# Kernel optimization log

Hardware: AMD Instinct MI355X
Metric: run time of the kernel (lower is better)

Reference implementation:

```python
import jax, jax.numpy as jnp
import numpy as np

N = 100000      # nodes
E = 3200000     # edges (before self loops)
IN = 128        # in_channels
H = 8           # heads
C = 16          # out_channels per head
NEG_SLOPE = 0.2


def setup_inputs() -> dict:
    key = jax.random.key(0)
    k1, k2, k3, k4, k5, k6 = jax.random.split(key, 6)
    x = jax.random.normal(k1, (N, IN), dtype=jnp.float32)
    edge_index = jax.random.randint(k2, (2, E), 0, N, dtype=jnp.int32)
    # GATConv params: lin weight [IN, H*C], att_src/att_dst [H, C], bias [H*C]
    W = jax.random.normal(k3, (IN, H * C), dtype=jnp.float32) / np.float32(np.sqrt(IN))
    att_src = jax.random.normal(k4, (H, C), dtype=jnp.float32) / np.float32(np.sqrt(C))
    att_dst = jax.random.normal(k5, (H, C), dtype=jnp.float32) / np.float32(np.sqrt(C))
    bias = jax.random.normal(k6, (H * C,), dtype=jnp.float32) * 0.01
    return {"x": x, "edge_index": edge_index, "W": W,
            "att_src": att_src, "att_dst": att_dst, "bias": bias}


def reference(x, edge_index, W, att_src, att_dst, bias):
    n = x.shape[0]
    h = (x @ W).reshape(n, H, C)                      # [N, H, C]
    # add self loops (PyG default add_self_loops=True)
    loop = jnp.arange(n, dtype=edge_index.dtype)
    src = jnp.concatenate([edge_index[0], loop])      # [E+N] message sources j
    dst = jnp.concatenate([edge_index[1], loop])      # [E+N] targets i
    # per-node attention logits
    a_src = jnp.einsum('nhc,hc->nh', h, att_src)      # [N, H]
    a_dst = jnp.einsum('nhc,hc->nh', h, att_dst)      # [N, H]
    alpha = jax.nn.leaky_relu(a_src[src] + a_dst[dst], NEG_SLOPE)  # [E+N, H]
    # segment softmax over edges grouped by destination node
    amax = jax.lax.stop_gradient(jax.ops.segment_max(alpha, dst, num_segments=n))
    ex = jnp.exp(alpha - amax[dst])
    denom = jax.ops.segment_sum(ex, dst, num_segments=n)           # [N, H]
    w = ex / (denom[dst] + 1e-16)                                  # [E+N, H]
    msg = h[src] * w[:, :, None]                                   # [E+N, H, C]
    out = jax.ops.segment_sum(msg, dst, num_segments=n)            # [N, H, C]
    return out.reshape(n, H * C) + bias
```

## Files before the change

### kernel.cpp

```cpp
#include <hip/hip_runtime.h>
#include <hip/hip_bf16.h>

#define H 8
#define C 16
#define HC 128
#define NEG 0.2f
#define XS_S 132

#define ANSH 6
#define AN 64
#define AMSK 63
#define CAP2 2560
#define MAXB2 2048
#define CB_SH 12
#define CBMSK 4095
#define MAXB1 64
#define EPB 4096

__device__ __forceinline__ float lrelu(float x) { return fmaxf(x, NEG * x); }

__device__ __forceinline__ unsigned pack_bf16(float a, float b) {
    union { __hip_bfloat16 h; unsigned short u; } ua, ub;
    ua.h = __float2bfloat16(a);
    ub.h = __float2bfloat16(b);
    return (unsigned)ua.u | ((unsigned)ub.u << 16);
}
__device__ __forceinline__ float bf_lo(unsigned d) { return __uint_as_float(d << 16); }
__device__ __forceinline__ float bf_hi(unsigned d) { return __uint_as_float(d & 0xffff0000u); }

__global__ void __launch_bounds__(256) k1_gemm(const float* __restrict__ x,
                                               const float* __restrict__ W,
                                               const float* __restrict__ att_src,
                                               const float* __restrict__ att_dst,
                                               unsigned* __restrict__ h16,
                                               float* __restrict__ a_src,
                                               float* __restrict__ a_dst, int N) {
    __shared__ float xs[64 * XS_S];
    const int n0 = blockIdx.x * 64;
    const int t = threadIdx.x;
#pragma unroll
    for (int i = 0; i < 8; ++i) {
        int id = t + 256 * i;
        int r = id >> 5, kq = id & 31;
        int n = n0 + r;
        float4 v = (n < N) ? ((const float4*)x)[(size_t)n * 32 + kq]
                           : make_float4(0.f, 0.f, 0.f, 0.f);
        *(float4*)&xs[r * XS_S + kq * 4] = v;
    }
    __syncthreads();
    const int cg = t & 31;
    const int r0 = (t >> 5) * 8;
    float acc[8][4];
#pragma unroll
    for (int i = 0; i < 8; ++i)
#pragma unroll
        for (int j = 0; j < 4; ++j) acc[i][j] = 0.f;

#pragma unroll 4
    for (int k = 0; k < HC; ++k) {
        const float4 wv = ((const float4*)W)[k * 32 + cg];
        float wr[4] = {wv.x, wv.y, wv.z, wv.w};
#pragma unroll
        for (int i = 0; i < 8; ++i) {
            float xv = xs[(r0 + i) * XS_S + k];
#pragma unroll
            for (int j = 0; j < 4; ++j) acc[i][j] += xv * wr[j];
        }
    }
    const int fhd = cg >> 2;
    const int cq  = cg & 3;
#pragma unroll
    for (int i = 0; i < 8; ++i) {
        int n = n0 + r0 + i;
        if (n < N) {
            uint2 dv = make_uint2(pack_bf16(acc[i][0], acc[i][1]),
                                  pack_bf16(acc[i][2], acc[i][3]));
            *(uint2*)&h16[(size_t)n * 64 + cg * 2] = dv;
        }
        float ps = 0.f, pd = 0.f;
#pragma unroll
        for (int jj = 0; jj < 4; ++jj) {
            float hv = acc[i][jj];
            ps += hv * att_src[fhd * C + cq * 4 + jj];
            pd += hv * att_dst[fhd * C + cq * 4 + jj];
        }
        ps += __shfl_xor(ps, 1, 4); pd += __shfl_xor(pd, 1, 4);
        ps += __shfl_xor(ps, 2, 4); pd += __shfl_xor(pd, 2, 4);
        if (cq == 0 && n < N) {
            a_src[(unsigned)n * 8u + fhd] = ps;
            a_dst[(unsigned)n * 8u + fhd] = pd;
        }
    }
}

__global__ void __launch_bounds__(256) kb_bin1(const int* __restrict__ ei,
                                               int* __restrict__ gcount1,
                                               unsigned* __restrict__ pairs1,
                                               int E, int NB1, int cap1) {
    __shared__ int hist[4][MAXB1];
    __shared__ int cur[4][MAXB1];
    __shared__ int tot[MAXB1];
    __shared__ int scn[MAXB1];
    const int t = threadIdx.x;
    const int wv = t >> 6;
    const int e0 = blockIdx.x * EPB;
    const int nE = min(EPB, E - e0);
    ((int*)hist)[t] = 0;
    __syncthreads();

    const bool al4 = ((E & 3) == 0);
    const int nE4 = nE >> 2;
    int4 dreg[4], sreg[4];
    const int4* d4p = (const int4*)(ei + E + e0);
    const int4* s4p = (const int4*)(ei + e0);
#pragma unroll
    for (int j = 0; j < 4; ++j) {
        int idx = j * 256 + t;
        if (idx < nE4) {
            if (al4) { dreg[j] = d4p[idx]; sreg[j] = s4p[idx]; }
            else {
                int e = idx * 4;
                dreg[j] = make_int4(ei[E + e0 + e], ei[E + e0 + e + 1],
                                    ei[E + e0 + e + 2], ei[E + e0 + e + 3]);
                sreg[j] = make_int4(ei[e0 + e], ei[e0 + e + 1],
                                    ei[e0 + e + 2], ei[e0 + e + 3]);
            }
        }
    }
    int tlD = 0, tlS = -1;
    {
        int tb = nE4 * 4 + t;
        if (tb < nE) { tlD = ei[E + e0 + tb]; tlS = ei[e0 + tb]; }
    }
#pragma unroll
    for (int j = 0; j < 4; ++j) {
        if (j * 256 + t < nE4) {
            atomicAdd(&hist[wv][dreg[j].x >> CB_SH], 1);
            atomicAdd(&hist[wv][dreg[j].y >> CB_SH], 1);
            atomicAdd(&hist[wv][dreg[j].z >> CB_SH], 1);
            atomicAdd(&hist[wv][dreg[j].w >> CB_SH], 1);
        }
    }
    if (tlS >= 0) atomicAdd(&hist[wv][tlD >> CB_SH], 1);
    __syncthreads();
    if (t < MAXB1) {
        int s = 0;
#pragma unroll
        for (int w = 0; w < 4; ++w) s += hist[w][t];
        tot[t] = s;
        scn[t] = s;
    }
    __syncthreads();
    for (int off = 1; off < MAXB1; off <<= 1) {
        int v = (t < MAXB1 && t >= off) ? scn[t - off] : 0;
        __syncthreads();
        if (t < MAXB1) scn[t] += v;
        __syncthreads();
    }
    if (t < MAXB1) {
        int h = tot[t];
        int gb = h ? t * cap1 + atomicAdd(&gcount1[t], h) : 0;
#pragma unroll
        for (int w = 0; w < 4; ++w) { cur[w][t] = gb; gb += hist[w][t]; }
    }
    __syncthreads();
#pragma unroll
    for (int j = 0; j < 4; ++j) {
        if (j * 256 + t < nE4) {
#pragma unroll
            for (int q = 0; q < 4; ++q) {
                int dst = (&dreg[j].x)[q], src = (&sreg[j].x)[q];
                int b = dst >> CB_SH;
                int pos = atomicAdd(&cur[wv][b], 1);
                if (pos < b * cap1 + cap1)
                    pairs1[pos] = (unsigned)src | ((unsigned)(dst & CBMSK) << 17);
            }
        }
    }
    if (tlS >= 0) {
        int b = tlD >> CB_SH;
        int pos = atomicAdd(&cur[wv][b], 1);
        if (pos < b * cap1 + cap1)
            pairs1[pos] = (unsigned)tlS | ((unsigned)(tlD & CBMSK) << 17);
    }
}

__global__ void __launch_bounds__(256) kb_bin2(const unsigned* __restrict__ pairs1,
                                               const int* __restrict__ gcount1,
                                               int* __restrict__ gcount2,
                                               unsigned* __restrict__ pairs2,
                                               int cap1, int ch2) {
    __shared__ int hist[4][64];
    __shared__ int cur[4][64];
    __shared__ int tot[64];
    const int cb = blockIdx.x / ch2;
    const int ci = blockIdx.x % ch2;
    const int c1 = min(gcount1[cb], cap1);
    const int e0 = ci * EPB;
    if (e0 >= c1) return;
    const int nE = min(EPB, c1 - e0);
    const unsigned b1 = (unsigned)cb * (unsigned)cap1 + (unsigned)e0;
    const int t = threadIdx.x;
    const int wv = t >> 6;
    ((int*)hist)[t] = 0;
    __syncthreads();

    const int nE4 = nE >> 2;
    const uint4* p4 = (const uint4*)(pairs1 + b1);
    uint4 preg[4];
#pragma unroll
    for (int j = 0; j < 4; ++j) {
        int idx = j * 256 + t;
        if (idx < nE4) preg[j] = p4[idx];
    }
    unsigned tlP = 0; int tlV = 0;
    {
        int tb = nE4 * 4 + t;
        if (tb < nE) { tlP = pairs1[b1 + tb]; tlV = 1; }
    }
#pragma unroll
    for (int j = 0; j < 4; ++j) {
        if (j * 256 + t < nE4) {
            atomicAdd(&hist[wv][preg[j].x >> 23], 1);
            atomicAdd(&hist[wv][preg[j].y >> 23], 1);
            atomicAdd(&hist[wv][preg[j].z >> 23], 1);
            atomicAdd(&hist[wv][preg[j].w >> 23], 1);
        }
    }
    if (tlV) atomicAdd(&hist[wv][tlP >> 23], 1);
    __syncthreads();
    if (t < 64) {
        int s = 0;
#pragma unroll
        for (int w = 0; w < 4; ++w) s += hist[w][t];
        tot[t] = s;
    }
    __syncthreads();
    if (t < 64) {
        int h = tot[t];
        int gfb = cb * 64 + t;
        int gb = h ? gfb * CAP2 + atomicAdd(&gcount2[gfb], h) : 0;
#pragma unroll
        for (int w = 0; w < 4; ++w) { cur[w][t] = gb; gb += hist[w][t]; }
    }
    __syncthreads();
#pragma unroll
    for (int j = 0; j < 4; ++j) {
        if (j * 256 + t < nE4) {
#pragma unroll
            for (int q = 0; q < 4; ++q) {
                unsigned pv = (&preg[j].x)[q];
                int fb = pv >> 23;
                int pos = atomicAdd(&cur[wv][fb], 1);
                if (pos < (cb * 64 + fb) * CAP2 + CAP2)
                    pairs2[pos] = (pv & 0x1FFFFu) | (((pv >> 17) & 63u) << 18);
            }
        }
    }
    if (tlV) {
        int fb = tlP >> 23;
        int pos = atomicAdd(&cur[wv][fb], 1);
        if (pos < (cb * 64 + fb) * CAP2 + CAP2)
            pairs2[pos] = (tlP & 0x1FFFFu) | (((tlP >> 17) & 63u) << 18);
    }
}

__global__ void __launch_bounds__(512) k_fused(const unsigned* __restrict__ pairs,
                                               const int* __restrict__ gcount,
                                               const unsigned* __restrict__ h16,
                                               const float* __restrict__ a_src,
                                               const float* __restrict__ a_dst,
                                               const float* __restrict__ bias,
                                               float* __restrict__ out, int N) {
    __shared__ int cnt[AN];
    __shared__ int sc[AN];
    __shared__ int lcur[AN];
    __shared__ int lbeg[AN + 1];
    __shared__ unsigned scol[CAP2];
    const int b = blockIdx.x;
    const int t = threadIdx.x;
    const int n0 = b << ANSH;
    const unsigned base = (unsigned)b * (unsigned)CAP2;
    const int cb = min(gcount[b], CAP2);

    if (t < AN) cnt[t] = 0;
    __syncthreads();
    for (int j = t; j < cb; j += 512)
        atomicAdd(&cnt[pairs[base + j] >> 18], 1);
    __syncthreads();
    if (t < AN) sc[t] = cnt[t];
    __syncthreads();
    for (int off = 1; off < AN; off <<= 1) {
        int v = (t < AN && t >= off) ? sc[t - off] : 0;
        __syncthreads();
        if (t < AN) sc[t] += v;
        __syncthreads();
    }
    if (t < AN) {
        lbeg[t + 1] = sc[t];
        lcur[t] = sc[t] - cnt[t];
        if (t == 0) lbeg[0] = 0;
    }
    __syncthreads();
    for (int j = t; j < cb; j += 512) {
        unsigned pv = pairs[base + j];
        int pos = atomicAdd(&lcur[pv >> 18], 1);
        scol[pos] = pv & 0x3FFFFu;
    }
    __syncthreads();

    const int wv = t >> 6;
    const int lane = t & 63;
    const int hd = lane >> 3;
    const int hw = lane & 7;
    const int bidx = hd * 4;

    for (int nl = wv; nl < AN; nl += 8) {
        const int node = n0 + nl;
        if (node >= N) break;
        const float adst_own = a_dst[(unsigned)node * 8u + (unsigned)hd];
        const float adst_hh  = a_dst[(unsigned)node * 8u + (unsigned)hw];
        const float wself = __expf(lrelu(a_src[(unsigned)node * 8u + (unsigned)hd] + adst_own));
        unsigned dself = h16[(unsigned)node * 64u + (unsigned)lane];
        float a0 = bf_lo(dself) * wself, a1 = bf_hi(dself) * wself;
        float b0 = 0.f, b1 = 0.f, c0 = 0.f, c1 = 0.f, e0 = 0.f, e1 = 0.f;
        float sA = wself, sB = 0.f, sC = 0.f, sD = 0.f;

        const int beg = lbeg[nl], end = lbeg[nl + 1];
        int j = beg;
        for (; j + 8 <= end; j += 8) {
            unsigned m0 = scol[j],     m1 = scol[j + 1], m2 = scol[j + 2], m3 = scol[j + 3];
            unsigned m4 = scol[j + 4], m5 = scol[j + 5], m6 = scol[j + 6], m7 = scol[j + 7];
            unsigned nP = scol[j + (lane >> 3)];
            float wme = __expf(lrelu(a_src[nP * 8u + (unsigned)hw] + adst_hh));
            int wi = __float_as_int(wme);
            float w0 = __int_as_float(__builtin_amdgcn_ds_bpermute(bidx,       wi));
            float w1 = __int_as_float(__builtin_amdgcn_ds_bpermute(bidx + 32,  wi));
            float w2 = __int_as_float(__builtin_amdgcn_ds_bpermute(bidx + 64,  wi));
            float w3 = __int_as_float(__builtin_amdgcn_ds_bpermute(bidx + 96,  wi));
            float w4 = __int_as_float(__builtin_amdgcn_ds_bpermute(bidx + 128, wi));
            float w5 = __int_as_float(__builtin_amdgcn_ds_bpermute(bidx + 160, wi));
            float w6 = __int_as_float(__builtin_amdgcn_ds_bpermute(bidx + 192, wi));
            float w7 = __int_as_float(__builtin_amdgcn_ds_bpermute(bidx + 224, wi));
            unsigned d0 = h16[m0 * 64u + (unsigned)lane];
            unsigned d1 = h16[m1 * 64u + (unsigned)lane];
            unsigned d2 = h16[m2 * 64u + (unsigned)lane];
            unsigned d3 = h16[m3 * 64u + (unsigned)lane];
            unsigned d4 = h16[m4 * 64u + (unsigned)lane];
            unsigned d5 = h16[m5 * 64u + (unsigned)lane];
            unsigned d6 = h16[m6 * 64u + (unsigned)lane];
            unsigned d7 = h16[m7 * 64u + (unsigned)lane];
            a0 += bf_lo(d0) * w0; a1 += bf_hi(d0) * w0; sA += w0;
            b0 += bf_lo(d1) * w1; b1 += bf_hi(d1) * w1; sB += w1;
            c0 += bf_lo(d2) * w2; c1 += bf_hi(d2) * w2; sC += w2;
            e0 += bf_lo(d3) * w3; e1 += bf_hi(d3) * w3; sD += w3;
            a0 += bf_lo(d4) * w4; a1 += bf_hi(d4) * w4; sA += w4;
            b0 += bf_lo(d5) * w5; b1 += bf_hi(d5) * w5; sB += w5;
            c0 += bf_lo(d6) * w6; c1 += bf_hi(d6) * w6; sC += w6;
            e0 += bf_lo(d7) * w7; e1 += bf_hi(d7) * w7; sD += w7;
        }
        if (j + 4 <= end) {
            unsigned m0 = scol[j], m1 = scol[j + 1], m2 = scol[j + 2], m3 = scol[j + 3];
            unsigned nP = scol[j + ((lane >> 3) & 3)];
            float wme = __expf(lrelu(a_src[nP * 8u + (unsigned)hw] + adst_hh));
            int wi = __float_as_int(wme);
            float w0 = __int_as_float(__builtin_amdgcn_ds_bpermute(bidx,      wi));
            float w1 = __int_as_float(__builtin_amdgcn_ds_bpermute(bidx + 32, wi));
            float w2 = __int_as_float(__builtin_amdgcn_ds_bpermute(bidx + 64, wi));
            float w3 = __int_as_float(__builtin_amdgcn_ds_bpermute(bidx + 96, wi));
            unsigned d0 = h16[m0 * 64u + (unsigned)lane];
            unsigned d1 = h16[m1 * 64u + (unsigned)lane];
            unsigned d2 = h16[m2 * 64u + (unsigned)lane];
            unsigned d3 = h16[m3 * 64u + (unsigned)lane];
            a0 += bf_lo(d0) * w0; a1 += bf_hi(d0) * w0; sA += w0;
            b0 += bf_lo(d1) * w1; b1 += bf_hi(d1) * w1; sB += w1;
            c0 += bf_lo(d2) * w2; c1 += bf_hi(d2) * w2; sC += w2;
            e0 += bf_lo(d3) * w3; e1 += bf_hi(d3) * w3; sD += w3;
            j += 4;
        }
        for (; j < end; ++j) {
            unsigned mA = scol[j];
            float wA = __expf(lrelu(a_src[mA * 8u + (unsigned)hd] + adst_own));
            unsigned dA = h16[mA * 64u + (unsigned)lane];
            a0 += bf_lo(dA) * wA; a1 += bf_hi(dA) * wA; sA += wA;
        }
        const float s = sA + sB + sC + sD;
        const float inv = 1.f / (s + 1e-16f);
        const float acc0 = a0 + b0 + c0 + e0;
        const float acc1 = a1 + b1 + c1 + e1;
        const float2 bv = ((const float2*)bias)[lane];
        float2 o;
        o.x = acc0 * inv + bv.x;
        o.y = acc1 * inv + bv.y;
        ((float2*)out)[(unsigned)node * 64u + (unsigned)lane] = o;
    }
}

extern "C" void kernel_launch(void* const* d_in, const int* in_sizes, int n_in,
                              void* d_out, int out_size, void* d_ws, size_t ws_size,
                              hipStream_t stream) {
    const float* x       = (const float*)d_in[0];
    const int*   ei      = (const int*)d_in[1];
    const float* W       = (const float*)d_in[2];
    const float* att_src = (const float*)d_in[3];
    const float* att_dst = (const float*)d_in[4];
    const float* bias    = (const float*)d_in[5];
    float* out = (float*)d_out;

    const int N = in_sizes[0] / HC;
    const int E = in_sizes[1] / 2;
    const int B = (N + AMSK) >> ANSH;
    const int NB1 = (N + CBMSK) >> CB_SH;
    const int nbin = (E + EPB - 1) / EPB;
    const int cap1 = (((E + NB1 - 1) / NB1) + 32768 + 3) & ~3;
    const int ch2 = (cap1 + EPB - 1) / EPB;

    unsigned* h16 = (unsigned*)d_ws;
    float* a_src  = (float*)(h16 + (size_t)N * 64);
    float* a_dst  = a_src + (size_t)N * H;
    int* gcount1  = (int*)(a_dst + (size_t)N * H);
    int* gcount2  = gcount1 + MAXB1;
    unsigned* pairs1 = (unsigned*)(gcount2 + MAXB2);
    unsigned* pairs2 = pairs1 + (size_t)NB1 * (size_t)cap1;

    (void)hipMemsetAsync(gcount1, 0, (MAXB1 + MAXB2) * sizeof(int), stream);
    kb_bin1<<<nbin, 256, 0, stream>>>(ei, gcount1, pairs1, E, NB1, cap1);
    kb_bin2<<<NB1 * ch2, 256, 0, stream>>>(pairs1, gcount1, gcount2, pairs2,
                                           cap1, ch2);
    k1_gemm<<<(N + 63) / 64, 256, 0, stream>>>(x, W, att_src, att_dst,
                                               h16, a_src, a_dst, N);
    k_fused<<<B, 512, 0, stream>>>(pairs2, gcount2, h16, a_src,
                                   a_dst, bias, out, N);
}
```

Measured before the change: 353.9 us.

## Sub-bucket edges by source range and aggregate in phases for gather locality

Within each destination block, edges are now counted and sorted by (destination node, source range of 16K nodes) with a 512-entry scan, then processed in eight phases separated by block barriers. Each phase gathers only h16 rows from one source range, so concurrent blocks touch a smaller working set and L2 hit rates may rise. Partial sums are kept in shared memory (an added 32KB float2 tile plus per-head sums) and finalized in a last pass with the self-loop term. The cost is eight extra barriers, a larger scan, shorter per-segment loops with a 4-wide unroll in place of 8, and higher LDS use, which may lower occupancy.

Result: slower. 426.7 us (+20.6%).

```diff
diff --git a/kernel.cpp b/kernel.cpp
--- a/kernel.cpp
+++ b/kernel.cpp
@@ -16,6 +16,8 @@
 #define CBMSK 4095
 #define MAXB1 64
 #define EPB 4096
+#define NTL 8
+#define TL_SH 14
 
 __device__ __forceinline__ float lrelu(float x) { return fmaxf(x, NEG * x); }
 
@@ -272,39 +274,42 @@
                                                const float* __restrict__ a_dst,
                                                const float* __restrict__ bias,
                                                float* __restrict__ out, int N) {
-    __shared__ int cnt[AN];
-    __shared__ int sc[AN];
-    __shared__ int lcur[AN];
-    __shared__ int lbeg[AN + 1];
+    __shared__ int cnt[AN * NTL];
+    __shared__ int sc[AN * NTL];
+    __shared__ int lcur[AN * NTL];
     __shared__ unsigned scol[CAP2];
+    __shared__ float2 st[AN * 64];
+    __shared__ float ssum[AN * 8];
     const int b = blockIdx.x;
     const int t = threadIdx.x;
     const int n0 = b << ANSH;
     const unsigned base = (unsigned)b * (unsigned)CAP2;
     const int cb = min(gcount[b], CAP2);
 
-    if (t < AN) cnt[t] = 0;
-    __syncthreads();
-    for (int j = t; j < cb; j += 512)
-        atomicAdd(&cnt[pairs[base + j] >> 18], 1);
-    __syncthreads();
-    if (t < AN) sc[t] = cnt[t];
-    __syncthreads();
-    for (int off = 1; off < AN; off <<= 1) {
-        int v = (t < AN && t >= off) ? sc[t - off] : 0;
-        __syncthreads();
-        if (t < AN) sc[t] += v;
-        __syncthreads();
-    }
-    if (t < AN) {
-        lbeg[t + 1] = sc[t];
-        lcur[t] = sc[t] - cnt[t];
-        if (t == 0) lbeg[0] = 0;
-    }
+    cnt[t] = 0;
+    ssum[t] = 0.f;
+    for (int i = t; i < AN * 64; i += 512) st[i] = make_float2(0.f, 0.f);
     __syncthreads();
     for (int j = t; j < cb; j += 512) {
         unsigned pv = pairs[base + j];
-        int pos = atomicAdd(&lcur[pv >> 18], 1);
+        int key = (int)((pv >> 18) * NTL + ((pv & 0x3FFFFu) >> TL_SH));
+        atomicAdd(&cnt[key], 1);
+    }
+    __syncthreads();
+    sc[t] = cnt[t];
+    __syncthreads();
+    for (int off = 1; off < AN * NTL; off <<= 1) {
+        int v = (t >= off) ? sc[t - off] : 0;
+        __syncthreads();
+        sc[t] += v;
+        __syncthreads();
+    }
+    lcur[t] = sc[t] - cnt[t];
+    __syncthreads();
+    for (int j = t; j < cb; j += 512) {
+        unsigned pv = pairs[base + j];
+        int key = (int)((pv >> 18) * NTL + ((pv & 0x3FFFFu) >> TL_SH));
+        int pos = atomicAdd(&lcur[key], 1);
         scol[pos] = pv & 0x3FFFFu;
     }
     __syncthreads();
@@ -315,83 +320,63 @@
     const int hw = lane & 7;
     const int bidx = hd * 4;
 
+    for (int s = 0; s < NTL; ++s) {
+        for (int nl = wv; nl < AN; nl += 8) {
+            const int key = nl * NTL + s;
+            const int beg = key ? sc[key - 1] : 0;
+            const int end = sc[key];
+            const int node = n0 + nl;
+            if (beg >= end || node >= N) continue;
+            float2 stv = st[nl * 64 + lane];
+            float sacc = 0.f;
+            const float adst_own = a_dst[(unsigned)node * 8u + (unsigned)hd];
+            const float adst_hh  = a_dst[(unsigned)node * 8u + (unsigned)hw];
+            int j = beg;
+            for (; j + 4 <= end; j += 4) {
+                unsigned m0 = scol[j], m1 = scol[j + 1];
+                unsigned m2 = scol[j + 2], m3 = scol[j + 3];
+                unsigned nP = scol[j + ((lane >> 3) & 3)];
+                float wme = __expf(lrelu(a_src[nP * 8u + (unsigned)hw] + adst_hh));
+                int wi = __float_as_int(wme);
+                float w0 = __int_as_float(__builtin_amdgcn_ds_bpermute(bidx,      wi));
+                float w1 = __int_as_float(__builtin_amdgcn_ds_bpermute(bidx + 32, wi));
+                float w2 = __int_as_float(__builtin_amdgcn_ds_bpermute(bidx + 64, wi));
+                float w3 = __int_as_float(__builtin_amdgcn_ds_bpermute(bidx + 96, wi));
+                unsigned d0 = h16[m0 * 64u + (unsigned)lane];
+                unsigned d1 = h16[m1 * 64u + (unsigned)lane];
+                unsigned d2 = h16[m2 * 64u + (unsigned)lane];
+                unsigned d3 = h16[m3 * 64u + (unsigned)lane];
+                stv.x += bf_lo(d0) * w0; stv.y += bf_hi(d0) * w0;
+                stv.x += bf_lo(d1) * w1; stv.y += bf_hi(d1) * w1;
+                stv.x += bf_lo(d2) * w2; stv.y += bf_hi(d2) * w2;
+                stv.x += bf_lo(d3) * w3; stv.y += bf_hi(d3) * w3;
+                sacc += w0 + w1 + w2 + w3;
+            }
+            for (; j < end; ++j) {
+                unsigned mA = scol[j];
+                float wA = __expf(lrelu(a_src[mA * 8u + (unsigned)hd] + adst_own));
+                unsigned dA = h16[mA * 64u + (unsigned)lane];
+                stv.x += bf_lo(dA) * wA; stv.y += bf_hi(dA) * wA;
+                sacc += wA;
+            }
+            st[nl * 64 + lane] = stv;
+            if ((lane & 7) == 0) ssum[nl * 8 + hd] += sacc;
+        }
+        __syncthreads();
+    }
+
     for (int nl = wv; nl < AN; nl += 8) {
         const int node = n0 + nl;
-        if (node >= N) break;
-        const float adst_own = a_dst[(unsigned)node * 8u + (unsigned)hd];
-        const float adst_hh  = a_dst[(unsigned)node * 8u + (unsigned)hw];
-        const float wself = __expf(lrelu(a_src[(unsigned)node * 8u + (unsigned)hd] + adst_own));
-        unsigned dself = h16[(unsigned)node * 64u + (unsigned)lane];
-        float a0 = bf_lo(dself) * wself, a1 = bf_hi(dself) * wself;
-        float b0 = 0.f, b1 = 0.f, c0 = 0.f, c1 = 0.f, e0 = 0.f, e1 = 0.f;
-        float sA = wself, sB = 0.f, sC = 0.f, sD = 0.f;
-
-        const int beg = lbeg[nl], end = lbeg[nl + 1];
-        int j = beg;
-        for (; j + 8 <= end; j += 8) {
-            unsigned m0 = scol[j],     m1 = scol[j + 1], m2 = scol[j + 2], m3 = scol[j + 3];
-            unsigned m4 = scol[j + 4], m5 = scol[j + 5], m6 = scol[j + 6], m7 = scol[j + 7];
-            unsigned nP = scol[j + (lane >> 3)];
-            float wme = __expf(lrelu(a_src[nP * 8u + (unsigned)hw] + adst_hh));
-            int wi = __float_as_int(wme);
-            float w0 = __int_as_float(__builtin_amdgcn_ds_bpermute(bidx,       wi));
-            float w1 = __int_as_float(__builtin_amdgcn_ds_bpermute(bidx + 32,  wi));
-            float w2 = __int_as_float(__builtin_amdgcn_ds_bpermute(bidx + 64,  wi));
-            float w3 = __int_as_float(__builtin_amdgcn_ds_bpermute(bidx + 96,  wi));
-            float w4 = __int_as_float(__builtin_amdgcn_ds_bpermute(bidx + 128, wi));
-            float w5 = __int_as_float(__builtin_amdgcn_ds_bpermute(bidx + 160, wi));
-            float w6 = __int_as_float(__builtin_amdgcn_ds_bpermute(bidx + 192, wi));
-            float w7 = __int_as_float(__builtin_amdgcn_ds_bpermute(bidx + 224, wi));
-            unsigned d0 = h16[m0 * 64u + (unsigned)lane];
-            unsigned d1 = h16[m1 * 64u + (unsigned)lane];
-            unsigned d2 = h16[m2 * 64u + (unsigned)lane];
-            unsigned d3 = h16[m3 * 64u + (unsigned)lane];
-            unsigned d4 = h16[m4 * 64u + (unsigned)lane];
-            unsigned d5 = h16[m5 * 64u + (unsigned)lane];
-            unsigned d6 = h16[m6 * 64u + (unsigned)lane];
-            unsigned d7 = h16[m7 * 64u + (unsigned)lane];
-            a0 += bf_lo(d0) * w0; a1 += bf_hi(d0) * w0; sA += w0;
-            b0 += bf_lo(d1) * w1; b1 += bf_hi(d1) * w1; sB += w1;
-            c0 += bf_lo(d2) * w2; c1 += bf_hi(d2) * w2; sC += w2;
-            e0 += bf_lo(d3) * w3; e1 += bf_hi(d3) * w3; sD += w3;
-            a0 += bf_lo(d4) * w4; a1 += bf_hi(d4) * w4; sA += w4;
-            b0 += bf_lo(d5) * w5; b1 += bf_hi(d5) * w5; sB += w5;
-            c0 += bf_lo(d6) * w6; c1 += bf_hi(d6) * w6; sC += w6;
-            e0 += bf_lo(d7) * w7; e1 += bf_hi(d7) * w7; sD += w7;
-        }
-        if (j + 4 <= end) {
-            unsigned m0 = scol[j], m1 = scol[j + 1], m2 = scol[j + 2], m3 = scol[j + 3];
-            unsigned nP = scol[j + ((lane >> 3) & 3)];
-            float wme = __expf(lrelu(a_src[nP * 8u + (unsigned)hw] + adst_hh));
-            int wi = __float_as_int(wme);
-            float w0 = __int_as_float(__builtin_amdgcn_ds_bpermute(bidx,      wi));
-            float w1 = __int_as_float(__builtin_amdgcn_ds_bpermute(bidx + 32, wi));
-            float w2 = __int_as_float(__builtin_amdgcn_ds_bpermute(bidx + 64, wi));
-            float w3 = __int_as_float(__builtin_amdgcn_ds_bpermute(bidx + 96, wi));
-            unsigned d0 = h16[m0 * 64u + (unsigned)lane];
-            unsigned d1 = h16[m1 * 64u + (unsigned)lane];
-            unsigned d2 = h16[m2 * 64u + (unsigned)lane];
-            unsigned d3 = h16[m3 * 64u + (unsigned)lane];
-            a0 += bf_lo(d0) * w0; a1 += bf_hi(d0) * w0; sA += w0;
-            b0 += bf_lo(d1) * w1; b1 += bf_hi(d1) * w1; sB += w1;
-            c0 += bf_lo(d2) * w2; c1 += bf_hi(d2) * w2; sC += w2;
-            e0 += bf_lo(d3) * w3; e1 += bf_hi(d3) * w3; sD += w3;
-            j += 4;
-        }
-        for (; j < end; ++j) {
-            unsigned mA = scol[j];
-            float wA = __expf(lrelu(a_src[mA * 8u + (unsigned)hd] + adst_own));
-            unsigned dA = h16[mA * 64u + (unsigned)lane];
-            a0 += bf_lo(dA) * wA; a1 += bf_hi(dA) * wA; sA += wA;
-        }
-        const float s = sA + sB + sC + sD;
-        const float inv = 1.f / (s + 1e-16f);
-        const float acc0 = a0 + b0 + c0 + e0;
-        const float acc1 = a1 + b1 + c1 + e1;
-        const float2 bv = ((const float2*)bias)[lane];
+        if (node >= N) continue;
+        float wself = __expf(lrelu(a_src[(unsigned)node * 8u + (unsigned)hd] +
+                                   a_dst[(unsigned)node * 8u + (unsigned)hd]));
+        unsigned dsf = h16[(unsigned)node * 64u + (unsigned)lane];
+        float2 stv = st[nl * 64 + lane];
+        float inv = 1.f / (ssum[nl * 8 + hd] + wself + 1e-16f);
+        float2 bv = ((const float2*)bias)[lane];
         float2 o;
-        o.x = acc0 * inv + bv.x;
-        o.y = acc1 * inv + bv.y;
+        o.x = (stv.x + bf_lo(dsf) * wself) * inv + bv.x;
+        o.y = (stv.y + bf_hi(dsf) * wself) * inv + bv.y;
         ((float2*)out)[(unsigned)node * 64u + (unsigned)lane] = o;
     }
 }
```
